# Kernel tuning notes

Hardware: AMD Instinct MI355X
Metric: run time of the kernel (lower is better)

The kernel has to match this reference:

```python
import jax, jax.numpy as jnp
import numpy as np

IN_FEATURES = 4096
PADDED_DIM = 4096           # == in_features -> pad and crop are identity
K_HALF = PADDED_DIM // 2 + 1  # 2049
K_KEEP = 1024               # low-pass mask: keep first K coefficients
BATCH = 8192


def _half_clean(H_real, H_imag):
    """Masked half-spectrum with real DC and Nyquist bins (padded_dim even)."""
    mask = (jnp.arange(K_HALF) < K_KEEP).astype(H_real.dtype)
    mask = jax.lax.stop_gradient(mask)
    hr = H_real * mask
    hi = H_imag * mask
    hi = hi.at[0].set(0.0)    # DC bin real
    hi = hi.at[-1].set(0.0)   # Nyquist bin real (padded_dim even, k_half > 1)
    return hr + 1j * hi


def setup_inputs() -> dict:
    key = jax.random.key(0)
    k1, k2, k3, k4 = jax.random.split(key, 4)
    x = jax.random.normal(k1, (BATCH, IN_FEATURES), jnp.float32)
    H_real = jax.random.normal(k2, (K_HALF,), jnp.float32) * 0.1
    H_imag = jax.random.normal(k3, (K_HALF,), jnp.float32) * 0.1
    bias = jax.random.normal(k4, (PADDED_DIM,), jnp.float32) * 0.1
    return {"x": x, "H_real": H_real, "H_imag": H_imag, "bias": bias}


def reference(x, H_real, H_imag, bias):
    # in_features == padded_dim, so no pad/crop needed.
    Xf = jnp.fft.rfft(x, axis=-1, norm="ortho")           # [B, K_HALF] complex64
    Yf = Xf * _half_clean(H_real, H_imag)                  # elementwise spectral multiply
    y = jnp.fft.irfft(Yf, n=PADDED_DIM, axis=-1, norm="ortho")  # [B, PADDED_DIM]
    y = y + bias[None, :]                                  # vector_bias=True
    return y
```

## Files before the change

kernel.cpp:

```cpp
#include <hip/hip_runtime.h>
#include <math.h>

#define NFEAT 4096
#define M     2048
#define THREADS 256
#define ROWS_PER_WG 4

#define SWZ(i) ((i) ^ (((i) >> 4) & 15))

__device__ __forceinline__ float2 cmul(float2 a, float2 b){
    return make_float2(a.x*b.x - a.y*b.y, a.x*b.y + a.y*b.x);
}
__device__ __forceinline__ float2 cadd(float2 a, float2 b){ return make_float2(a.x+b.x, a.y+b.y); }
__device__ __forceinline__ float2 csub(float2 a, float2 b){ return make_float2(a.x-b.x, a.y-b.y); }

template<int SIGN>
__device__ __forceinline__ void fft4(float2& a0, float2& a1, float2& a2, float2& a3){
    float2 t0 = cadd(a0,a2), t1 = csub(a0,a2);
    float2 t2 = cadd(a1,a3), t3 = csub(a1,a3);
    float2 r3 = (SIGN < 0) ? make_float2(t3.y, -t3.x) : make_float2(-t3.y, t3.x);
    a0 = cadd(t0,t2); a2 = csub(t0,t2);
    a1 = cadd(t1,r3); a3 = csub(t1,r3);
}

template<int SIGN>
__device__ __forceinline__ void fft8(float2 v[8]){
    const float C = 0.70710678118654752440f;
    float2 e0=v[0], e1=v[2], e2=v[4], e3=v[6];
    float2 o0=v[1], o1=v[3], o2=v[5], o3=v[7];
    fft4<SIGN>(e0,e1,e2,e3);
    fft4<SIGN>(o0,o1,o2,o3);
    float2 w1 = make_float2( C, (SIGN<0) ? -C : C);
    float2 w3 = make_float2(-C, (SIGN<0) ? -C : C);
    float2 o1w = cmul(o1, w1);
    float2 o2w = (SIGN<0) ? make_float2(o2.y, -o2.x) : make_float2(-o2.y, o2.x);
    float2 o3w = cmul(o3, w3);
    v[0]=cadd(e0,o0);  v[4]=csub(e0,o0);
    v[1]=cadd(e1,o1w); v[5]=csub(e1,o1w);
    v[2]=cadd(e2,o2w); v[6]=csub(e2,o2w);
    v[3]=cadd(e3,o3w); v[7]=csub(e3,o3w);
}

template<int SIGN, int NS>
__device__ __forceinline__ void stage8(const float2* __restrict__ src, float2* __restrict__ dst,
                                       const float2* __restrict__ tw, int j){
    const int m  = j & (NS - 1);
    const int tb = m * (M / (NS * 8));
    float2 v[8];
#pragma unroll
    for (int r = 0; r < 8; ++r){
        float2 a = src[SWZ(j + 256*r)];
        if (NS == 1 || r == 0){
            v[r] = a;
        } else {
            int tt = tb * r;
            float2 w = tw[tt & 1023];
            float s = (tt & 1024) ? -1.f : 1.f;
            w.x *= s;
            w.y = (SIGN < 0) ? w.y * s : -w.y * s;
            v[r] = cmul(a, w);
        }
    }
    fft8<SIGN>(v);
    const int idxD = ((j - m) << 3) + m;
#pragma unroll
    for (int r = 0; r < 8; ++r)
        dst[SWZ(idxD + NS*r)] = v[r];
}

template<int SIGN, int NS>
__device__ __forceinline__ void stage4(const float2* __restrict__ src, float2* __restrict__ dst,
                                       const float2* __restrict__ tw, int j){
    const int m  = j & (NS - 1);
    const int tb = m * (M / (NS * 4));
    float2 v[4];
#pragma unroll
    for (int r = 0; r < 4; ++r){
        float2 a = src[SWZ(j + 512*r)];
        if (r == 0){ v[r] = a; }
        else {
            int tt = tb * r;
            float2 w = tw[tt & 1023];
            float s = (tt & 1024) ? -1.f : 1.f;
            w.x *= s;
            w.y = (SIGN < 0) ? w.y * s : -w.y * s;
            v[r] = cmul(a, w);
        }
    }
    fft4<SIGN>(v[0], v[1], v[2], v[3]);
    const int idxD = ((j - m) << 2) + m;
#pragma unroll
    for (int r = 0; r < 4; ++r)
        dst[SWZ(idxD + NS*r)] = v[r];
}

extern "C" __global__ void __launch_bounds__(THREADS)
rfft_circ_kernel(const float* __restrict__ x,
                 const float* __restrict__ Hr,
                 const float* __restrict__ Hi,
                 const float* __restrict__ bias,
                 float* __restrict__ out)
{
    __shared__ float2 bufA[M];
    __shared__ float2 bufB[M];
    __shared__ float2 tw1[1024];
    __shared__ float2 tw2[1024];

    const int t = threadIdx.x;

    for (int i = t; i < 1024; i += THREADS){
        float s, c;
        sincosf(-6.2831853071795864769f * (float)i * (1.0f/2048.0f), &s, &c);
        tw1[i] = make_float2(c, s);
        sincosf(-6.2831853071795864769f * (float)i * (1.0f/4096.0f), &s, &c);
        tw2[i] = make_float2(c, s);
    }
    __syncthreads();

#pragma unroll 1
    for (int rr = 0; rr < ROWS_PER_WG; ++rr){
        const int row = blockIdx.x * ROWS_PER_WG + rr;
        const float4* xr = (const float4*)(x + (size_t)row * NFEAT);

#pragma unroll
        for (int q = 0; q < 4; ++q){
            int u = t + THREADS*q;
            float4 d = xr[u];
            bufA[SWZ(2*u)]   = make_float2(d.x, d.y);
            bufA[SWZ(2*u+1)] = make_float2(d.z, d.w);
        }
        __syncthreads();

        stage8<-1,1  >(bufA, bufB, tw1, t); __syncthreads();
        stage8<-1,8  >(bufB, bufA, tw1, t); __syncthreads();
        stage8<-1,64 >(bufA, bufB, tw1, t); __syncthreads();
        stage4<-1,512>(bufB, bufA, tw1, t);
        stage4<-1,512>(bufB, bufA, tw1, t + 256);
        __syncthreads();

#pragma unroll
        for (int q = 0; q < 4; ++q){
            int k = t + THREADS*q;
            if (k == 0){
                float2 z0 = bufA[SWZ(0)];
                float X0 = z0.x + z0.y;
                float Y0 = X0 * Hr[0];
                bufB[SWZ(0)]    = make_float2(0.5f*Y0, 0.5f*Y0);
                bufB[SWZ(1024)] = make_float2(0.f, 0.f);
            } else {
                float2 zk = bufA[SWZ(k)];
                float2 zm = bufA[SWZ(2048 - k)];
                float2 w  = tw2[k];
                float2 A = make_float2(0.5f*(zk.x + zm.x), 0.5f*(zk.y - zm.y));
                float2 B = make_float2(0.5f*(zk.x - zm.x), 0.5f*(zk.y + zm.y));
                float2 wB = cmul(w, B);
                float2 X = make_float2(A.x + wB.y, A.y - wB.x);
                float2 H = make_float2(Hr[k], Hi[k]);
                float2 Y = cmul(X, H);
                float2 f1 = make_float2(1.f + w.y,  w.x);
                float2 f2 = make_float2(1.f - w.y,  w.x);
                float2 Yc = make_float2(Y.x, -Y.y);
                float2 zy1 = cmul(Y,  f1);
                float2 zy2 = cmul(Yc, f2);
                bufB[SWZ(k)]        = make_float2(0.5f*zy1.x, 0.5f*zy1.y);
                bufB[SWZ(2048 - k)] = make_float2(0.5f*zy2.x, 0.5f*zy2.y);
            }
        }
        __syncthreads();

        stage8<1,1  >(bufB, bufA, tw1, t); __syncthreads();
        stage8<1,8  >(bufA, bufB, tw1, t); __syncthreads();
        stage8<1,64 >(bufB, bufA, tw1, t); __syncthreads();
        stage4<1,512>(bufA, bufB, tw1, t);
        stage4<1,512>(bufA, bufB, tw1, t + 256);
        __syncthreads();

        float4* yr = (float4*)(out + (size_t)row * NFEAT);
        const float4* br = (const float4*)bias;
        const float inv = (1.0f/2048.0f);
#pragma unroll
        for (int q = 0; q < 4; ++q){
            int u = t + THREADS*q;
            float2 z0 = bufB[SWZ(2*u)];
            float2 z1 = bufB[SWZ(2*u+1)];
            float4 b = br[u];
            float4 o;
            o.x = fmaf(z0.x, inv, b.x);
            o.y = fmaf(z0.y, inv, b.y);
            o.z = fmaf(z1.x, inv, b.z);
            o.w = fmaf(z1.y, inv, b.w);
            yr[u] = o;
        }
        __syncthreads();
    }
}

extern "C" void kernel_launch(void* const* d_in, const int* in_sizes, int n_in,
                              void* d_out, int out_size, void* d_ws, size_t ws_size,
                              hipStream_t stream) {
    const float* x    = (const float*)d_in[0];
    const float* Hr   = (const float*)d_in[1];
    const float* Hi   = (const float*)d_in[2];
    const float* bias = (const float*)d_in[3];
    float* out        = (float*)d_out;

    const int n_rows = in_sizes[0] / NFEAT;
    dim3 grid(n_rows / ROWS_PER_WG), block(THREADS);
    hipLaunchKernelGGL(rfft_circ_kernel, grid, block, 0, stream,
                       x, Hr, Hi, bias, out);
}
```

Baseline: 283.4 us.

## Fuse first FFT stage into global load and last stage into store

Runs the first radix-8 stage directly on registers loaded from global memory, and the final radix-4 stage directly before the global store with the bias add. This removes one LDS round trip and one barrier at each end of the row pipeline. It also merges the two twiddle tables into one quarter-wave swizzled table that derives the 2048-point twiddles by symmetry, which cuts LDS use. The price is narrower float2 global accesses instead of float4, plus extra select logic per twiddle.

```diff
diff --git a/kernel.cpp b/kernel.cpp
--- a/kernel.cpp
+++ b/kernel.cpp
@@ -7,12 +7,23 @@
 #define ROWS_PER_WG 4
 
 #define SWZ(i) ((i) ^ (((i) >> 4) & 15))
+#define TWPHYS(e) ((e) ^ (((e) >> 4) & 15))
 
 __device__ __forceinline__ float2 cmul(float2 a, float2 b){
     return make_float2(a.x*b.x - a.y*b.y, a.x*b.y + a.y*b.x);
 }
 __device__ __forceinline__ float2 cadd(float2 a, float2 b){ return make_float2(a.x+b.x, a.y+b.y); }
 __device__ __forceinline__ float2 csub(float2 a, float2 b){ return make_float2(a.x-b.x, a.y-b.y); }
+
+template<int SIGN>
+__device__ __forceinline__ float2 tw2048(const float2* __restrict__ twq, int tt){
+    int e = (tt & 511) << 1;
+    float2 w = twq[TWPHYS(e)];
+    if (tt & 512)  w = make_float2(w.y, -w.x);
+    if (tt & 1024) w = make_float2(-w.x, -w.y);
+    if (SIGN > 0)  w.y = -w.y;
+    return w;
+}
 
 template<int SIGN>
 __device__ __forceinline__ void fft4(float2& a0, float2& a1, float2& a2, float2& a3){
@@ -43,54 +54,20 @@
 
 template<int SIGN, int NS>
 __device__ __forceinline__ void stage8(const float2* __restrict__ src, float2* __restrict__ dst,
-                                       const float2* __restrict__ tw, int j){
+                                       const float2* __restrict__ twq, int j){
     const int m  = j & (NS - 1);
     const int tb = m * (M / (NS * 8));
     float2 v[8];
 #pragma unroll
     for (int r = 0; r < 8; ++r){
         float2 a = src[SWZ(j + 256*r)];
-        if (NS == 1 || r == 0){
-            v[r] = a;
-        } else {
-            int tt = tb * r;
-            float2 w = tw[tt & 1023];
-            float s = (tt & 1024) ? -1.f : 1.f;
-            w.x *= s;
-            w.y = (SIGN < 0) ? w.y * s : -w.y * s;
-            v[r] = cmul(a, w);
-        }
+        if (NS == 1 || r == 0) v[r] = a;
+        else                   v[r] = cmul(a, tw2048<SIGN>(twq, tb * r));
     }
     fft8<SIGN>(v);
     const int idxD = ((j - m) << 3) + m;
 #pragma unroll
     for (int r = 0; r < 8; ++r)
-        dst[SWZ(idxD + NS*r)] = v[r];
-}
-
-template<int SIGN, int NS>
-__device__ __forceinline__ void stage4(const float2* __restrict__ src, float2* __restrict__ dst,
-                                       const float2* __restrict__ tw, int j){
-    const int m  = j & (NS - 1);
-    const int tb = m * (M / (NS * 4));
-    float2 v[4];
-#pragma unroll
-    for (int r = 0; r < 4; ++r){
-        float2 a = src[SWZ(j + 512*r)];
-        if (r == 0){ v[r] = a; }
-        else {
-            int tt = tb * r;
-            float2 w = tw[tt & 1023];
-            float s = (tt & 1024) ? -1.f : 1.f;
-            w.x *= s;
-            w.y = (SIGN < 0) ? w.y * s : -w.y * s;
-            v[r] = cmul(a, w);
-        }
-    }
-    fft4<SIGN>(v[0], v[1], v[2], v[3]);
-    const int idxD = ((j - m) << 2) + m;
-#pragma unroll
-    for (int r = 0; r < 4; ++r)
         dst[SWZ(idxD + NS*r)] = v[r];
 }
 
@@ -103,39 +80,49 @@
 {
     __shared__ float2 bufA[M];
     __shared__ float2 bufB[M];
-    __shared__ float2 tw1[1024];
-    __shared__ float2 tw2[1024];
+    __shared__ float2 twq[1024];
 
     const int t = threadIdx.x;
 
     for (int i = t; i < 1024; i += THREADS){
         float s, c;
-        sincosf(-6.2831853071795864769f * (float)i * (1.0f/2048.0f), &s, &c);
-        tw1[i] = make_float2(c, s);
         sincosf(-6.2831853071795864769f * (float)i * (1.0f/4096.0f), &s, &c);
-        tw2[i] = make_float2(c, s);
+        twq[TWPHYS(i)] = make_float2(c, s);
     }
     __syncthreads();
 
 #pragma unroll 1
     for (int rr = 0; rr < ROWS_PER_WG; ++rr){
         const int row = blockIdx.x * ROWS_PER_WG + rr;
-        const float4* xr = (const float4*)(x + (size_t)row * NFEAT);
-
-#pragma unroll
-        for (int q = 0; q < 4; ++q){
-            int u = t + THREADS*q;
-            float4 d = xr[u];
-            bufA[SWZ(2*u)]   = make_float2(d.x, d.y);
-            bufA[SWZ(2*u+1)] = make_float2(d.z, d.w);
+        const float2* xr2 = (const float2*)(x + (size_t)row * NFEAT);
+
+        {
+            float2 v[8];
+#pragma unroll
+            for (int r = 0; r < 8; ++r) v[r] = xr2[t + 256*r];
+            fft8<-1>(v);
+            const int idxD = t << 3;
+#pragma unroll
+            for (int r = 0; r < 8; ++r) bufB[SWZ(idxD + r)] = v[r];
         }
         __syncthreads();
 
-        stage8<-1,1  >(bufA, bufB, tw1, t); __syncthreads();
-        stage8<-1,8  >(bufB, bufA, tw1, t); __syncthreads();
-        stage8<-1,64 >(bufA, bufB, tw1, t); __syncthreads();
-        stage4<-1,512>(bufB, bufA, tw1, t);
-        stage4<-1,512>(bufB, bufA, tw1, t + 256);
+        stage8<-1,8 >(bufB, bufA, twq, t); __syncthreads();
+        stage8<-1,64>(bufA, bufB, twq, t); __syncthreads();
+
+#pragma unroll
+        for (int h = 0; h < 2; ++h){
+            const int j = t + 256*h;
+            float2 v0 = bufB[SWZ(j)];
+            float2 v1 = cmul(bufB[SWZ(j +  512)], tw2048<-1>(twq, j));
+            float2 v2 = cmul(bufB[SWZ(j + 1024)], tw2048<-1>(twq, 2*j));
+            float2 v3 = cmul(bufB[SWZ(j + 1536)], tw2048<-1>(twq, 3*j));
+            fft4<-1>(v0,v1,v2,v3);
+            bufA[SWZ(j)]        = v0;
+            bufA[SWZ(j +  512)] = v1;
+            bufA[SWZ(j + 1024)] = v2;
+            bufA[SWZ(j + 1536)] = v3;
+        }
         __syncthreads();
 
 #pragma unroll
@@ -150,7 +137,7 @@
             } else {
                 float2 zk = bufA[SWZ(k)];
                 float2 zm = bufA[SWZ(2048 - k)];
-                float2 w  = tw2[k];
+                float2 w  = twq[TWPHYS(k)];
                 float2 A = make_float2(0.5f*(zk.x + zm.x), 0.5f*(zk.y - zm.y));
                 float2 B = make_float2(0.5f*(zk.x - zm.x), 0.5f*(zk.y + zm.y));
                 float2 wB = cmul(w, B);
@@ -168,30 +155,32 @@
         }
         __syncthreads();
 
-        stage8<1,1  >(bufB, bufA, tw1, t); __syncthreads();
-        stage8<1,8  >(bufA, bufB, tw1, t); __syncthreads();
-        stage8<1,64 >(bufB, bufA, tw1, t); __syncthreads();
-        stage4<1,512>(bufA, bufB, tw1, t);
-        stage4<1,512>(bufA, bufB, tw1, t + 256);
-        __syncthreads();
-
-        float4* yr = (float4*)(out + (size_t)row * NFEAT);
-        const float4* br = (const float4*)bias;
+        stage8<1,1 >(bufB, bufA, twq, t); __syncthreads();
+        stage8<1,8 >(bufA, bufB, twq, t); __syncthreads();
+        stage8<1,64>(bufB, bufA, twq, t); __syncthreads();
+
+        float2* yr2 = (float2*)(out + (size_t)row * NFEAT);
+        const float2* br2 = (const float2*)bias;
         const float inv = (1.0f/2048.0f);
 #pragma unroll
-        for (int q = 0; q < 4; ++q){
-            int u = t + THREADS*q;
-            float2 z0 = bufB[SWZ(2*u)];
-            float2 z1 = bufB[SWZ(2*u+1)];
-            float4 b = br[u];
-            float4 o;
-            o.x = fmaf(z0.x, inv, b.x);
-            o.y = fmaf(z0.y, inv, b.y);
-            o.z = fmaf(z1.x, inv, b.z);
-            o.w = fmaf(z1.y, inv, b.w);
-            yr[u] = o;
-        }
-        __syncthreads();
+        for (int h = 0; h < 2; ++h){
+            const int j = t + 256*h;
+            float2 v0 = bufA[SWZ(j)];
+            float2 v1 = cmul(bufA[SWZ(j +  512)], tw2048<1>(twq, j));
+            float2 v2 = cmul(bufA[SWZ(j + 1024)], tw2048<1>(twq, 2*j));
+            float2 v3 = cmul(bufA[SWZ(j + 1536)], tw2048<1>(twq, 3*j));
+            fft4<1>(v0,v1,v2,v3);
+            float2 vv[4] = {v0,v1,v2,v3};
+#pragma unroll
+            for (int r = 0; r < 4; ++r){
+                int mo = j + 512*r;
+                float2 b = br2[mo];
+                float2 o;
+                o.x = fmaf(vv[r].x, inv, b.x);
+                o.y = fmaf(vv[r].y, inv, b.y);
+                yr2[mo] = o;
+            }
+        }
     }
 }
 
```

Measured after the change: 271.9 us. 4.1% less time.
